# Performance work log

Measured on AMD Instinct MI355X. Metric: run time of the kernel, lower is better.

The kernel has to match this reference:

```python
import jax, jax.numpy as jnp
import numpy as np

D_MODEL = 1024
D_STATE = 16
D_CONV = 4
EXPAND = 2
D_INNER = EXPAND * D_MODEL  # 2048
DT_RANK = 64  # ceil(1024/16)
BATCH = 2
SEQ = 1024
EPS = 1e-5


def _causal_depthwise_conv(x, w, b):
    # x: (B, L, D); w: (D, K) depthwise kernel; b: (D,)
    K = w.shape[1]
    xp = jnp.pad(x, ((0, 0), (K - 1, 0), (0, 0)))            # left-pad for causality
    out = jax.lax.conv_general_dilated(
        xp.transpose(0, 2, 1),          # (B, D, L+K-1)
        w[:, None, :],                  # (D, 1, K)
        window_strides=(1,), padding='VALID',
        feature_group_count=w.shape[0])
    return out.transpose(0, 2, 1) + b   # (B, L, D)


def _ssm_dir(xs, conv_w, conv_b, xproj_w, dt_w, dt_b, A_log, D_skip):
    # xs: (B, L, D_INNER)
    Bsz = xs.shape[0]
    xc = jax.nn.silu(_causal_depthwise_conv(xs, conv_w, conv_b))
    x_dbl = xc @ xproj_w                                        # (B, L, dt_rank + 2N)
    dt, B_ssm, C_ssm = jnp.split(x_dbl, [DT_RANK, DT_RANK + D_STATE], axis=-1)
    dt = jax.nn.softplus(dt @ dt_w + dt_b)                      # (B, L, D_INNER)
    A = -jnp.exp(A_log)                                         # (D_INNER, N)
    dA = jnp.exp(dt[..., None] * A)                             # (B, L, D_INNER, N)
    dBu = dt[..., None] * B_ssm[:, :, None, :] * xc[..., None]  # (B, L, D_INNER, N)

    def step(h, inp):
        dAt, dBut, ct = inp          # (B,D,N), (B,D,N), (B,N)
        h = dAt * h + dBut
        y = jnp.einsum('bdn,bn->bd', h, ct)
        return h, y

    h0 = jnp.zeros((Bsz, D_INNER, D_STATE), dtype=xs.dtype)
    _, ys = jax.lax.scan(step, h0,
                         (jnp.moveaxis(dA, 1, 0), jnp.moveaxis(dBu, 1, 0), jnp.moveaxis(C_ssm, 1, 0)))
    y = jnp.moveaxis(ys, 0, 1)                                  # (B, L, D_INNER)
    return y + xc * D_skip


def _layernorm(x, gamma, beta):
    mu = jnp.mean(x, axis=-1, keepdims=True)
    var = jnp.mean(jnp.square(x - mu), axis=-1, keepdims=True)
    return (x - mu) * jax.lax.rsqrt(var + EPS) * gamma + beta


def setup_inputs() -> dict:
    key = jax.random.key(0)
    ks = jax.random.split(key, 24)
    s = 0.02
    A_init = jnp.log(jnp.tile(jnp.arange(1, D_STATE + 1, dtype=jnp.float32)[None, :], (D_INNER, 1)))
    # dt bias init (inverse-softplus of small dt), as in the torch module
    dt0 = jnp.exp(jax.random.uniform(ks[20], (D_INNER,)) * (np.log(0.1) - np.log(0.001)) + np.log(0.001))
    dt0 = jnp.clip(dt0, 1e-4)
    inv_dt = dt0 + jnp.log(-jnp.expm1(-dt0))
    return {
        'x': jax.random.normal(ks[0], (BATCH, SEQ, D_MODEL), jnp.float32),
        'gamma': jnp.ones((D_MODEL,), jnp.float32),
        'beta': jnp.zeros((D_MODEL,), jnp.float32),
        'in_w': jax.random.normal(ks[1], (D_MODEL, 2 * D_INNER), jnp.float32) * s,
        'conv_w': jax.random.normal(ks[2], (D_INNER, D_CONV), jnp.float32) * s,
        'conv_b': jnp.zeros((D_INNER,), jnp.float32),
        'xproj_w': jax.random.normal(ks[3], (D_INNER, DT_RANK + 2 * D_STATE), jnp.float32) * s,
        'dt_w': jax.random.normal(ks[4], (DT_RANK, D_INNER), jnp.float32) * s,
        'dt_b': inv_dt,
        'A_log': A_init,
        'D_skip': jnp.ones((D_INNER,), jnp.float32),
        'conv_w_b': jax.random.normal(ks[5], (D_INNER, D_CONV), jnp.float32) * s,
        'conv_b_b': jnp.zeros((D_INNER,), jnp.float32),
        'xproj_w_b': jax.random.normal(ks[6], (D_INNER, DT_RANK + 2 * D_STATE), jnp.float32) * s,
        'dt_w_b': jax.random.normal(ks[7], (DT_RANK, D_INNER), jnp.float32) * s,
        'dt_b_b': inv_dt,
        'A_log_b': A_init,
        'D_skip_b': jnp.ones((D_INNER,), jnp.float32),
        'merge_w': jax.random.normal(ks[8], (2 * D_INNER, D_INNER), jnp.float32) * s,
        'out_w': jax.random.normal(ks[9], (D_INNER, D_MODEL), jnp.float32) * s,
    }


def reference(x, gamma, beta, in_w, conv_w, conv_b, xproj_w, dt_w, dt_b, A_log, D_skip,
              conv_w_b, conv_b_b, xproj_w_b, dt_w_b, dt_b_b, A_log_b, D_skip_b,
              merge_w, out_w):
    residual = x
    h = _layernorm(x, gamma, beta)
    xz = h @ in_w                               # (B, L, 2*D_INNER)
    xs, z = jnp.split(xz, 2, axis=-1)
    y_fwd = _ssm_dir(xs, conv_w, conv_b, xproj_w, dt_w, dt_b, A_log, D_skip)
    y_back = _ssm_dir(xs[:, ::-1], conv_w_b, conv_b_b, xproj_w_b, dt_w_b, dt_b_b, A_log_b, D_skip_b)[:, ::-1]
    y = jnp.concatenate([y_fwd, y_back], axis=-1) @ merge_w
    y = y * jax.nn.silu(z)
    y = y @ out_w
    return residual + y
```

## Files before the change

### kernel.cpp

```cpp
#include <hip/hip_runtime.h>
#include <hip/hip_bf16.h>
#include <math.h>

typedef __hip_bfloat16 bf16;
typedef unsigned int u32;
typedef __attribute__((ext_vector_type(8))) short bf16x8;
typedef __attribute__((ext_vector_type(4))) float f32x4;

#define BATCH 2
#define SEQ 1024
#define DM 1024
#define DI 2048
#define NST 16
#define DTR 64
#define XDN 96
#define XDP_LD 128
#define T_TOK 2048
#define N2 4096
#define NCHUNK 32
#define CLEN 32

static __device__ __forceinline__ float b2f(bf16 v) { return __bfloat162float(v); }
static __device__ __forceinline__ float bits2f(unsigned short u) {
    return __uint_as_float(((unsigned)u) << 16);
}

static __device__ __forceinline__ float softplus_fast(float t) {
    return (t > 20.f) ? t : __logf(1.f + __expf(t));
}

static __device__ __forceinline__ void gload_lds16(const void* g, void* l) {
    __builtin_amdgcn_global_load_lds((__attribute__((address_space(1))) u32*)(size_t)g,
                                     (__attribute__((address_space(3))) u32*)l, 16, 0, 0);
}

#define SBAR() do { asm volatile("" ::: "memory"); __builtin_amdgcn_s_barrier(); asm volatile("" ::: "memory"); } while (0)

static __device__ void tileT(const float* __restrict__ in, bf16* __restrict__ out,
                             int K, int N, int t, float (*tb)[33]) {
    int nt = N >> 5;
    int bx = (t % nt) << 5, by = (t / nt) << 5;
    int tx = threadIdx.x & 31, r0 = threadIdx.x >> 5;
#pragma unroll
    for (int r = r0; r < 32; r += 8)
        tb[r][tx] = in[(size_t)(by + r) * N + bx + tx];
    __syncthreads();
#pragma unroll
    for (int r = r0; r < 32; r += 8)
        out[(size_t)(bx + r) * K + by + tx] = __float2bfloat16(tb[tx][r]);
}

#define LN_BLKS   T_TOK
#define INW_T     ((N2 / 32) * (DM / 32))
#define OUTW_T    ((DM / 32) * (DI / 32))
#define MRGW_T    ((DI / 32) * (N2 / 32))
#define SMALL_BLK ((2 * XDP_LD * DI + 2 * DI * DTR) / 256)

__global__ __launch_bounds__(256) void prep_mega(const float* __restrict__ x,
                                                 const float* __restrict__ gamma,
                                                 const float* __restrict__ beta,
                                                 bf16* __restrict__ H,
                                                 const float* __restrict__ in_w, bf16* __restrict__ in_wT,
                                                 const float* __restrict__ out_w, bf16* __restrict__ out_wT,
                                                 const float* __restrict__ merge_w, bf16* __restrict__ merge_wT,
                                                 const float* __restrict__ xpf, const float* __restrict__ xpb,
                                                 bf16* __restrict__ XPF, bf16* __restrict__ XPB,
                                                 const float* __restrict__ dtwf, const float* __restrict__ dtwb,
                                                 bf16* __restrict__ dtwT) {
    __shared__ float tbuf[32][33];
    __shared__ float red[8];
    int bid = blockIdx.x;
    int tid = threadIdx.x;

    if (bid < LN_BLKS) {
        int t = bid;
        float xv[4];
        float s = 0.f, s2 = 0.f;
#pragma unroll
        for (int k = 0; k < 4; ++k) {
            float v = x[(size_t)t * DM + k * 256 + tid];
            xv[k] = v; s += v; s2 += v * v;
        }
#pragma unroll
        for (int off = 32; off; off >>= 1) {
            s  += __shfl_down(s, off);
            s2 += __shfl_down(s2, off);
        }
        int wid = tid >> 6, lane = tid & 63;
        if (!lane) { red[wid] = s; red[4 + wid] = s2; }
        __syncthreads();
        if (tid == 0) {
            float S = red[0] + red[1] + red[2] + red[3];
            float S2 = red[4] + red[5] + red[6] + red[7];
            float mu = S * (1.f / DM);
            float var = S2 * (1.f / DM) - mu * mu;
            red[0] = mu;
            red[1] = rsqrtf(var + 1e-5f);
        }
        __syncthreads();
        float mu = red[0], rs = red[1];
#pragma unroll
        for (int k = 0; k < 4; ++k) {
            int i = k * 256 + tid;
            H[(size_t)t * DM + i] = __float2bfloat16((xv[k] - mu) * rs * gamma[i] + beta[i]);
        }
        return;
    }
    bid -= LN_BLKS;
    if (bid < INW_T)  { tileT(in_w, in_wT, DM, N2, bid, tbuf); return; }
    bid -= INW_T;
    if (bid < OUTW_T) { tileT(out_w, out_wT, DI, DM, bid, tbuf); return; }
    bid -= OUTW_T;
    if (bid < MRGW_T) { tileT(merge_w, merge_wT, N2, DI, bid, tbuf); return; }
    bid -= MRGW_T;
    int idx = bid * 256 + tid;
    if (idx < 2 * XDP_LD * DI) {
        int dir = idx >= XDP_LD * DI;
        int i = idx - dir * (XDP_LD * DI);
        int n = i >> 11;
        int k = i & (DI - 1);
        float v = (n < XDN) ? (dir ? xpb : xpf)[k * XDN + n] : 0.f;
        (dir ? XPB : XPF)[i] = __float2bfloat16(v);
    } else {
        int j = idx - 2 * XDP_LD * DI;
        int dir = j >= DI * DTR;
        int e = j - dir * (DI * DTR);
        int n = e >> 6;
        int k = e & 63;
        dtwT[(size_t)dir * DI * DTR + n * DTR + k] =
            __float2bfloat16((dir ? dtwb : dtwf)[(size_t)k * DI + n]);
    }
}

template <int EPI>
__global__ __launch_bounds__(256) void mfma_gemm(const bf16* __restrict__ A,
                                                 const bf16* __restrict__ BT,
                                                 const bf16* __restrict__ BT2, int bysplit,
                                                 bf16* __restrict__ Cb,
                                                 const float* __restrict__ resid,
                                                 float* __restrict__ outf,
                                                 bf16* __restrict__ Pb,
                                                 const float* __restrict__ bias1,
                                                 const float* __restrict__ bias2,
                                                 int M, int N, int K) {
    __shared__ bf16 As[8192];
    __shared__ bf16 Bs[8192];
    int tid = threadIdx.x;
    int wave = tid >> 6, lane = tid & 63;
    int q = lane >> 4, ln16 = lane & 15;
    int bm = blockIdx.y * 128, bn = blockIdx.x * 128;
    int wm = (wave >> 1) * 64, wn = (wave & 1) * 64;
    const bf16* Bt = ((int)blockIdx.y < bysplit) ? BT : BT2;

    int ks = K / gridDim.z;
    int kb = blockIdx.z * ks;

    f32x4 zf; zf[0] = zf[1] = zf[2] = zf[3] = 0.f;
    f32x4 acc[4][4];
#pragma unroll
    for (int i = 0; i < 4; ++i)
#pragma unroll
        for (int j = 0; j < 4; ++j) acc[i][j] = zf;

    for (int k0 = kb; k0 < kb + ks; k0 += 64) {
#pragma unroll
        for (int i = 0; i < 4; ++i) {
            int s = wave * 256 + i * 64 + lane;
            int kg = s >> 7, m = s & 127;
            gload_lds16(&A[(size_t)(bm + m) * K + k0 + kg * 8], &As[(wave * 256 + i * 64) * 8]);
            gload_lds16(&Bt[(size_t)(bn + m) * K + k0 + kg * 8], &Bs[(wave * 256 + i * 64) * 8]);
        }
        __syncthreads();
#pragma unroll
        for (int kk = 0; kk < 2; ++kk) {
            bf16x8 af[4], bfr[4];
#pragma unroll
            for (int i = 0; i < 4; ++i) {
                af[i]  = *(const bf16x8*)&As[(((kk * 4 + q) * 128) + (wm + i * 16 + ln16)) * 8];
                bfr[i] = *(const bf16x8*)&Bs[(((kk * 4 + q) * 128) + (wn + i * 16 + ln16)) * 8];
            }
#pragma unroll
            for (int i = 0; i < 4; ++i)
#pragma unroll
                for (int j = 0; j < 4; ++j)
                    acc[i][j] = __builtin_amdgcn_mfma_f32_16x16x32_bf16(af[i], bfr[j], acc[i][j], 0, 0, 0);
        }
        __syncthreads();
    }

    size_t pbase = (size_t)blockIdx.z * M * N;
#pragma unroll
    for (int i = 0; i < 4; ++i)
#pragma unroll
        for (int r = 0; r < 4; ++r) {
            int row = bm + wm + i * 16 + q * 4 + r;
            const float* bias = (EPI == 4) ? ((row < T_TOK) ? bias1 : bias2) : nullptr;
#pragma unroll
            for (int j = 0; j < 4; ++j) {
                int col = bn + wn + j * 16 + ln16;
                size_t idx = (size_t)row * N + col;
                float v = acc[i][j][r];
                if (EPI == 0)      Cb[idx] = __float2bfloat16(v);
                else if (EPI == 1) outf[idx] = resid[idx] + v;
                else if (EPI == 2) outf[idx] = v;
                else if (EPI == 3) Pb[pbase + idx] = __float2bfloat16(v);
                else {
                    Cb[idx] = __float2bfloat16(softplus_fast(v + bias[col]));
                }
            }
        }
}

template <int EPI>
__global__ __launch_bounds__(512, 2) void gemm256(const bf16* __restrict__ A,
                                                  const bf16* __restrict__ BT,
                                                  bf16* __restrict__ Cb,
                                                  bf16* __restrict__ Pb,
                                                  int M, int N, int K) {
    __shared__ bf16 LA[4][8192];
    __shared__ bf16 LB[4][8192];
    int tid = threadIdx.x;
    int wave = tid >> 6, lane = tid & 63;
    int q = lane >> 4, ln16 = lane & 15;

    int gx = gridDim.x, gy = gridDim.y, gz = gridDim.z;
    int L = blockIdx.x + gx * (blockIdx.y + gy * blockIdx.z);
    int nwg = gx * gy * gz;
    int qd = nwg >> 3, rd = nwg & 7;
    int xcd = L & 7, base = L >> 3;
    int wg = (xcd < rd ? xcd * (qd + 1) : rd * (qd + 1) + (xcd - rd) * qd) + base;
    int bxi = wg % gx, byi = (wg / gx) % gy, bzi = wg / (gx * gy);

    int bm = byi * 256, bn = bxi * 256;
    int wm = (wave >> 2) * 128, wn = (wave & 3) * 64;
    int ksz = K / gz;
    int kb = bzi * ksz;
    int NT = ksz >> 5;

    int o0 = tid * 16, o1 = 8192 + tid * 16;
    int r0 = o0 >> 6, r1 = o1 >> 6;
    int c0 = (o0 & 63) ^ (((r0 >> 1) & 3) << 4);
    int c1 = (o1 & 63) ^ (((r1 >> 1) & 3) << 4);
    const bf16* pa0 = &A[(size_t)(bm + r0) * K + kb + (c0 >> 1)];
    const bf16* pa1 = &A[(size_t)(bm + r1) * K + kb + (c1 >> 1)];
    const bf16* pb0 = &BT[(size_t)(bn + r0) * K + kb + (c0 >> 1)];
    const bf16* pb1 = &BT[(size_t)(bn + r1) * K + kb + (c1 >> 1)];
    int d0 = wave * 512;
    int d1 = 4096 + wave * 512;

    int aoff[8], boff[4];
#pragma unroll
    for (int i = 0; i < 8; ++i) {
        int r = wm + i * 16 + ln16;
        aoff[i] = (r * 64 + q * 16) ^ (((r >> 1) & 3) << 4);
    }
#pragma unroll
    for (int j = 0; j < 4; ++j) {
        int r = wn + j * 16 + ln16;
        boff[j] = (r * 64 + q * 16) ^ (((r >> 1) & 3) << 4);
    }

    f32x4 zf; zf[0] = zf[1] = zf[2] = zf[3] = 0.f;
    f32x4 acc[8][4];
#pragma unroll
    for (int i = 0; i < 8; ++i)
#pragma unroll
        for (int j = 0; j < 4; ++j) acc[i][j] = zf;

    auto STAGE = [&](int b, int koff) {
        gload_lds16(pa0 + koff, &LA[b][d0]);
        gload_lds16(pa1 + koff, &LA[b][d1]);
        gload_lds16(pb0 + koff, &LB[b][d0]);
        gload_lds16(pb1 + koff, &LB[b][d1]);
    };

#define RD_FRAGS(AV, BV, TT) do {                                             \
        const bf16* LAb_ = LA[(TT) & 3];                                      \
        const bf16* LBb_ = LB[(TT) & 3];                                      \
        _Pragma("unroll")                                                     \
        for (int j_ = 0; j_ < 4; ++j_) BV[j_] = *(const bf16x8*)&LBb_[boff[j_] >> 1]; \
        _Pragma("unroll")                                                     \
        for (int i_ = 0; i_ < 8; ++i_) AV[i_] = *(const bf16x8*)&LAb_[aoff[i_] >> 1]; \
    } while (0)

#define MFMA_ALL(AV, BV) do {                                                 \
        __builtin_amdgcn_s_setprio(1);                                        \
        _Pragma("unroll")                                                     \
        for (int i_ = 0; i_ < 8; ++i_)                                        \
            _Pragma("unroll")                                                 \
            for (int j_ = 0; j_ < 4; ++j_)                                    \
                acc[i_][j_] = __builtin_amdgcn_mfma_f32_16x16x32_bf16(AV[i_], BV[j_], acc[i_][j_], 0, 0, 0); \
        __builtin_amdgcn_s_setprio(0);                                        \
    } while (0)

    bf16x8 avX[8], bvX[4], avY[8], bvY[4];

    STAGE(0, 0); STAGE(1, 32); STAGE(2, 64);
    asm volatile("s_waitcnt vmcnt(4)" ::: "memory");
    SBAR();
    RD_FRAGS(avX, bvX, 0);

    for (int t = 0; t < NT; t += 2) {
        if (t + 1 < NT) RD_FRAGS(avY, bvY, t + 1);
        if (t + 3 < NT) STAGE((t + 3) & 3, (t + 3) * 32);
        MFMA_ALL(avX, bvX);
        if (t + 3 < NT)      asm volatile("s_waitcnt vmcnt(4)" ::: "memory");
        else if (t + 2 < NT) asm volatile("s_waitcnt vmcnt(0)" ::: "memory");
        SBAR();
        if (t + 2 < NT) RD_FRAGS(avX, bvX, t + 2);
        if (t + 4 < NT) STAGE((t + 4) & 3, (t + 4) * 32);
        MFMA_ALL(avY, bvY);
        if (t + 4 < NT)      asm volatile("s_waitcnt vmcnt(4)" ::: "memory");
        else if (t + 3 < NT) asm volatile("s_waitcnt vmcnt(0)" ::: "memory");
        SBAR();
    }
#undef RD_FRAGS
#undef MFMA_ALL

    size_t pbase = (size_t)bzi * ((size_t)M * N);
#pragma unroll
    for (int i = 0; i < 8; ++i)
#pragma unroll
        for (int r = 0; r < 4; ++r) {
            int row = bm + wm + i * 16 + q * 4 + r;
#pragma unroll
            for (int j = 0; j < 4; ++j) {
                int col = bn + wn + j * 16 + ln16;
                size_t idx = (size_t)row * N + col;
                float v = acc[i][j][r];
                if (EPI == 0) Cb[idx] = __float2bfloat16(v);
                else          Pb[pbase + idx] = __float2bfloat16(v);
            }
        }
}

__global__ __launch_bounds__(256) void reduce_plain(const bf16* __restrict__ P, int ns, size_t MN,
                                                    bf16* __restrict__ O) {
    size_t i = ((size_t)blockIdx.x * 256 + threadIdx.x) * 4;
    float s[4] = {0.f, 0.f, 0.f, 0.f};
    for (int k = 0; k < ns; ++k) {
        ushort4 p = *reinterpret_cast<const ushort4*>(&P[(size_t)k * MN + i]);
        s[0] += bits2f(p.x); s[1] += bits2f(p.y); s[2] += bits2f(p.z); s[3] += bits2f(p.w);
    }
    bf16 r[4];
#pragma unroll
    for (int j = 0; j < 4; ++j) r[j] = __float2bfloat16(s[j]);
    *reinterpret_cast<ushort4*>(&O[i]) = *reinterpret_cast<ushort4*>(r);
}

__global__ __launch_bounds__(256) void reduce_gate(const bf16* __restrict__ P, int ns, size_t MN,
                                                   const bf16* __restrict__ XZ, bf16* __restrict__ YM) {
    size_t i = ((size_t)blockIdx.x * 256 + threadIdx.x) * 4;
    float s[4] = {0.f, 0.f, 0.f, 0.f};
    for (int k = 0; k < ns; ++k) {
        ushort4 p = *reinterpret_cast<const ushort4*>(&P[(size_t)k * MN + i]);
        s[0] += bits2f(p.x); s[1] += bits2f(p.y); s[2] += bits2f(p.z); s[3] += bits2f(p.w);
    }
    int t = (int)(i >> 11), c = (int)(i & (DI - 1));
    const bf16* zp = &XZ[(size_t)t * N2 + DI + c];
    bf16 r[4];
#pragma unroll
    for (int j = 0; j < 4; ++j) {
        float z = b2f(zp[j]);
        r[j] = __float2bfloat16(s[j] * (z / (1.f + __expf(-z))));
    }
    *reinterpret_cast<ushort4*>(&YM[i]) = *reinterpret_cast<ushort4*>(r);
}

__global__ __launch_bounds__(256) void reduce_out(const bf16* __restrict__ P, int ns, size_t MN,
                                                  const float* __restrict__ x, float* __restrict__ out) {
    size_t i = ((size_t)blockIdx.x * 256 + threadIdx.x) * 4;
    float s[4] = {0.f, 0.f, 0.f, 0.f};
    for (int k = 0; k < ns; ++k) {
        ushort4 p = *reinterpret_cast<const ushort4*>(&P[(size_t)k * MN + i]);
        s[0] += bits2f(p.x); s[1] += bits2f(p.y); s[2] += bits2f(p.z); s[3] += bits2f(p.w);
    }
    float4 xv = *reinterpret_cast<const float4*>(&x[i]);
    float4 o = {s[0] + xv.x, s[1] + xv.y, s[2] + xv.z, s[3] + xv.w};
    *reinterpret_cast<float4*>(&out[i]) = o;
}

__global__ __launch_bounds__(256) void reduce_xdbl(const bf16* __restrict__ P, int ns, size_t MN,
                                                   float* __restrict__ XDP, bf16* __restrict__ XDdt) {
    size_t i = ((size_t)blockIdx.x * 256 + threadIdx.x) * 4;
    float s[4] = {0.f, 0.f, 0.f, 0.f};
    for (int k = 0; k < ns; ++k) {
        ushort4 p = *reinterpret_cast<const ushort4*>(&P[(size_t)k * MN + i]);
        s[0] += bits2f(p.x); s[1] += bits2f(p.y); s[2] += bits2f(p.z); s[3] += bits2f(p.w);
    }
    float4 o = {s[0], s[1], s[2], s[3]};
    *reinterpret_cast<float4*>(&XDP[i]) = o;
    int col = (int)(i & (XDP_LD - 1));
    if (col < DTR) {
        size_t row = i >> 7;
        bf16 r[4];
#pragma unroll
        for (int j = 0; j < 4; ++j) r[j] = __float2bfloat16(s[j]);
        *reinterpret_cast<ushort4*>(&XDdt[row * DTR + col]) = *reinterpret_cast<ushort4*>(r);
    }
}

__global__ __launch_bounds__(256) void gemm_dt(const float* __restrict__ A,
                                               const float* __restrict__ Bw,
                                               const float* __restrict__ bias,
                                               bf16* __restrict__ Cb, int M, int N) {
    __shared__ float As[16][68];
    __shared__ float Bs[16][68];
    int tid = threadIdx.x;
    int bm = blockIdx.y * 64, bn = blockIdx.x * 64;
    int tx = tid & 15, ty = tid >> 4;
    float acc[4][4];
#pragma unroll
    for (int i = 0; i < 4; ++i)
#pragma unroll
        for (int j = 0; j < 4; ++j) acc[i][j] = 0.f;
    int arow = tid >> 2, acg = (tid & 3) * 4;
    int brow = tid >> 4, bcol = (tid & 15) * 4;
    for (int k0 = 0; k0 < DTR; k0 += 16) {
        float4 av = *reinterpret_cast<const float4*>(&A[(size_t)(bm + arow) * XDP_LD + k0 + acg]);
        As[acg + 0][arow] = av.x; As[acg + 1][arow] = av.y;
        As[acg + 2][arow] = av.z; As[acg + 3][arow] = av.w;
        float4 bv = *reinterpret_cast<const float4*>(&Bw[(size_t)(k0 + brow) * N + bn + bcol]);
        Bs[brow][bcol + 0] = bv.x; Bs[brow][bcol + 1] = bv.y;
        Bs[brow][bcol + 2] = bv.z; Bs[brow][bcol + 3] = bv.w;
        __syncthreads();
#pragma unroll
        for (int kk = 0; kk < 16; ++kk) {
            float4 a = *reinterpret_cast<const float4*>(&As[kk][ty * 4]);
            float4 b = *reinterpret_cast<const float4*>(&Bs[kk][tx * 4]);
            acc[0][0] += a.x * b.x; acc[0][1] += a.x * b.y; acc[0][2] += a.x * b.z; acc[0][3] += a.x * b.w;
            acc[1][0] += a.y * b.x; acc[1][1] += a.y * b.y; acc[1][2] += a.y * b.z; acc[1][3] += a.y * b.w;
            acc[2][0] += a.z * b.x; acc[2][1] += a.z * b.y; acc[2][2] += a.z * b.z; acc[2][3] += a.z * b.w;
            acc[3][0] += a.w * b.x; acc[3][1] += a.w * b.y; acc[3][2] += a.w * b.z; acc[3][3] += a.w * b.w;
        }
        __syncthreads();
    }
    int row0 = bm + ty * 4, col0 = bn + tx * 4;
#pragma unroll
    for (int i = 0; i < 4; ++i)
#pragma unroll
        for (int j = 0; j < 4; ++j) {
            float v = acc[i][j] + bias[col0 + j];
            Cb[(size_t)(row0 + i) * N + col0 + j] = __float2bfloat16(softplus_fast(v));
        }
}

__global__ __launch_bounds__(256) void conv_kernel(const bf16* __restrict__ XZ,
                                                   const float* __restrict__ wf, const float* __restrict__ bf_,
                                                   const float* __restrict__ wb, const float* __restrict__ bb_,
                                                   bf16* __restrict__ XCF, bf16* __restrict__ XCB) {
    int idx = blockIdx.x * 256 + threadIdx.x;
    int c = idx & (DI - 1);
    int g = idx >> 11;
    int l = g & (SEQ - 1);
    int b = g >> 10;
    float sf = bf_[c];
    float sb = bb_[c];
#pragma unroll
    for (int j = 0; j < 4; ++j) {
        int lf = l - 3 + j;
        if (lf >= 0) sf += wf[c * 4 + j] * b2f(XZ[((size_t)(b * SEQ + lf)) * N2 + c]);
        int lb = l + 3 - j;
        if (lb < SEQ) sb += wb[c * 4 + j] * b2f(XZ[((size_t)(b * SEQ + lb)) * N2 + c]);
    }
    XCF[idx] = __float2bfloat16(sf / (1.f + __expf(-sf)));
    XCB[idx] = __float2bfloat16(sb / (1.f + __expf(-sb)));
}

template <bool FINAL>
__global__ __launch_bounds__(256) void scan_chunk(const bf16* __restrict__ DTF_, const bf16* __restrict__ DTB_,
                                                  const bf16* __restrict__ XCF_, const bf16* __restrict__ XCB_,
                                                  const float* __restrict__ XDP,
                                                  const float* __restrict__ Af, const float* __restrict__ Ab,
                                                  const float* __restrict__ Df, const float* __restrict__ Db,
                                                  float* __restrict__ HLOC, float* __restrict__ SUMDT,
                                                  bf16* __restrict__ YCAT) {
    __shared__ float bsl[CLEN][32];
    int tid = threadIdx.x;
    int sg = tid & 1;
    int c = blockIdx.x * 128 + (tid >> 1);
    int b = blockIdx.y;
    int dir = blockIdx.z >> 5, chunk = blockIdx.z & 31;
    {
        int it = tid >> 3, j4 = (tid & 7) * 4;
        int sit = chunk * CLEN + it;
        int l = dir ? (SEQ - 1 - sit) : sit;
        size_t row = (size_t)dir * T_TOK + (size_t)b * SEQ + l;
        *(float4*)&bsl[it][j4] = *(const float4*)&XDP[row * XDP_LD + DTR + j4];
    }
    const bf16* DT = dir ? DTB_ : DTF_;
    const bf16* XC = dir ? XCB_ : XCF_;
    const float* Al = dir ? Ab : Af;
    float A[8];
#pragma unroll
    for (int n = 0; n < 8; ++n) A[n] = -__expf(Al[c * NST + sg * 8 + n]);
    size_t base = ((((size_t)dir * BATCH + b) * NCHUNK + chunk) * DI + c);
    float h[8];
    float Dv = 0.f;
    if (FINAL) {
#pragma unroll
        for (int n = 0; n < 8; ++n) h[n] = HLOC[base * NST + sg * 8 + n];
        Dv = (dir ? Db : Df)[c];
    } else {
#pragma unroll
        for (int n = 0; n < 8; ++n) h[n] = 0.f;
    }
    __syncthreads();
    float sumdt = 0.f;
    for (int it = 0; it < CLEN; ++it) {
        int sit = chunk * CLEN + it;
        int l = dir ? (SEQ - 1 - sit) : sit;
        size_t g = (size_t)b * SEQ + l;
        float dt = b2f(DT[g * DI + c]);
        float xc = b2f(XC[g * DI + c]);
        float dtxc = dt * xc;
        const float* bs = &bsl[it][sg * 8];
        if (FINAL) {
            float y = 0.f;
#pragma unroll
            for (int n = 0; n < 8; ++n) {
                h[n] = __expf(dt * A[n]) * h[n] + dtxc * bs[n];
                y += h[n] * bs[NST + n];
            }
            y += __shfl_xor(y, 1);
            if (!sg) YCAT[g * N2 + dir * DI + c] = __float2bfloat16(y + xc * Dv);
        } else {
            sumdt += dt;
#pragma unroll
            for (int n = 0; n < 8; ++n)
                h[n] = __expf(dt * A[n]) * h[n] + dtxc * bs[n];
        }
    }
    if (!FINAL) {
#pragma unroll
        for (int n = 0; n < 8; ++n) HLOC[base * NST + sg * 8 + n] = h[n];
        if (!sg) SUMDT[base] = sumdt;
    }
}

__global__ __launch_bounds__(256) void scan_combine(float* __restrict__ HLOC,
                                                    const float* __restrict__ SUMDT,
                                                    const float* __restrict__ Af,
                                                    const float* __restrict__ Ab) {
    int idx = blockIdx.x * 256 + threadIdx.x;
    int n = idx & 15;
    int c = (idx >> 4) & (DI - 1);
    int b = (idx >> 15) & 1;
    int dir = idx >> 16;
    float A = -__expf((dir ? Ab : Af)[c * NST + n]);
    float h = 0.f;
    for (int k = 0; k < NCHUNK; ++k) {
        size_t base = ((((size_t)dir * BATCH + b) * NCHUNK + k) * DI + c);
        float P = __expf(A * SUMDT[base]);
        float hl = HLOC[base * NST + n];
        HLOC[base * NST + n] = h;
        h = P * h + hl;
    }
}

__global__ __launch_bounds__(256) void gate_kernel(bf16* __restrict__ YM, const bf16* __restrict__ XZ) {
    int idx = blockIdx.x * 256 + threadIdx.x;
    int t = idx >> 11;
    int c = idx & (DI - 1);
    float z = b2f(XZ[(size_t)t * N2 + DI + c]);
    float y = b2f(YM[idx]);
    YM[idx] = __float2bfloat16(y * (z / (1.f + __expf(-z))));
}

extern "C" void kernel_launch(void* const* d_in, const int* in_sizes, int n_in,
                              void* d_out, int out_size, void* d_ws, size_t ws_size,
                              hipStream_t stream) {
    const float* x       = (const float*)d_in[0];
    const float* gamma   = (const float*)d_in[1];
    const float* beta    = (const float*)d_in[2];
    const float* in_w    = (const float*)d_in[3];
    const float* conv_w  = (const float*)d_in[4];
    const float* conv_b  = (const float*)d_in[5];
    const float* xproj_w = (const float*)d_in[6];
    const float* dt_w    = (const float*)d_in[7];
    const float* dt_b    = (const float*)d_in[8];
    const float* A_log   = (const float*)d_in[9];
    const float* D_skip  = (const float*)d_in[10];
    const float* conv_w_b  = (const float*)d_in[11];
    const float* conv_b_b  = (const float*)d_in[12];
    const float* xproj_w_b = (const float*)d_in[13];
    const float* dt_w_b    = (const float*)d_in[14];
    const float* dt_b_b    = (const float*)d_in[15];
    const float* A_log_b   = (const float*)d_in[16];
    const float* D_skip_b  = (const float*)d_in[17];
    const float* merge_w   = (const float*)d_in[18];
    const float* out_w     = (const float*)d_in[19];
    float* out = (float*)d_out;

    char* w = (char*)d_ws;
    size_t off = 0;
    bf16* H       = (bf16*)(w + off); off += (size_t)T_TOK * DM * 2;
    bf16* XZ      = (bf16*)(w + off); off += (size_t)T_TOK * N2 * 2;
    bf16* XCF     = (bf16*)(w + off); off += (size_t)T_TOK * DI * 2;
    bf16* XCB     = (bf16*)(w + off); off += (size_t)T_TOK * DI * 2;
    bf16* XPF     = (bf16*)(w + off); off += (size_t)XDP_LD * DI * 2;
    bf16* XPB     = (bf16*)(w + off); off += (size_t)XDP_LD * DI * 2;
    float* XDP    = (float*)(w + off); off += (size_t)2 * T_TOK * XDP_LD * 4;
    bf16* DTF     = (bf16*)(w + off); off += (size_t)T_TOK * DI * 2;
    bf16* DTB     = (bf16*)(w + off); off += (size_t)T_TOK * DI * 2;
    bf16* YCAT    = (bf16*)(w + off); off += (size_t)T_TOK * N2 * 2;
    bf16* in_wT   = (bf16*)(w + off); off += (size_t)N2 * DM * 2;
    bf16* out_wT  = (bf16*)(w + off); off += (size_t)DM * DI * 2;
    bf16* merge_wT= (bf16*)(w + off); off += (size_t)DI * N2 * 2;
    bf16* dtwT    = (bf16*)(w + off); off += (size_t)2 * DI * DTR * 2;
    bf16* XDdt    = (bf16*)(w + off); off += (size_t)2 * T_TOK * DTR * 2;
    char* PART = w + off;
    size_t avail = (ws_size > off) ? ws_size - off : 0;

    float* HLOC  = (float*)PART;
    float* SUMDT = (float*)(PART + (size_t)2 * BATCH * NCHUNK * DI * NST * 4);
    bf16* Pb     = (bf16*)PART;
    bf16* YM     = DTF;

    size_t MNm = (size_t)T_TOK * DI;
    size_t MNo = (size_t)T_TOK * DM;
    size_t MNx = (size_t)2 * T_TOK * XDP_LD;
    size_t MNz = (size_t)T_TOK * N2;
    int s_merge = (avail >= 4 * MNm * 2) ? 4 : (avail >= 2 * MNm * 2) ? 2 : 0;
    int s_out   = (avail >= 4 * MNo * 2) ? 4 : (avail >= 2 * MNo * 2) ? 2 : 0;
    int s_xdbl  = (avail >= 16 * MNx * 2) ? 16 : (avail >= 8 * MNx * 2) ? 8 : (avail >= 4 * MNx * 2) ? 4 : 0;
    int s_xz    = (avail >= 2 * MNz * 2) ? 2 : 0;

    prep_mega<<<LN_BLKS + INW_T + OUTW_T + MRGW_T + SMALL_BLK, 256, 0, stream>>>(
        x, gamma, beta, H, in_w, in_wT, out_w, out_wT, merge_w, merge_wT,
        xproj_w, xproj_w_b, XPF, XPB, dt_w, dt_w_b, dtwT);
    if (s_xz) {
        gemm256<3><<<dim3(N2 / 256, T_TOK / 256, s_xz), 512, 0, stream>>>(
            H, in_wT, nullptr, Pb, T_TOK, N2, DM);
        reduce_plain<<<(int)(MNz / 4 / 256), 256, 0, stream>>>(Pb, s_xz, MNz, XZ);
    } else {
        mfma_gemm<0><<<dim3(N2 / 128, T_TOK / 128), 256, 0, stream>>>(
            H, in_wT, in_wT, 1 << 30, XZ, nullptr, nullptr, nullptr, nullptr, nullptr, T_TOK, N2, DM);
    }
    conv_kernel<<<(T_TOK * DI) / 256, 256, 0, stream>>>(XZ, conv_w, conv_b, conv_w_b, conv_b_b, XCF, XCB);
    if (s_xdbl) {
        mfma_gemm<3><<<dim3(1, (2 * T_TOK) / 128, s_xdbl), 256, 0, stream>>>(
            XCF, XPF, XPB, (T_TOK / 128), nullptr, nullptr, nullptr, Pb, nullptr, nullptr,
            2 * T_TOK, XDP_LD, DI);
        reduce_xdbl<<<(int)(MNx / 4 / 256), 256, 0, stream>>>(Pb, s_xdbl, MNx, XDP, XDdt);
        mfma_gemm<4><<<dim3(DI / 128, (2 * T_TOK) / 128), 256, 0, stream>>>(
            XDdt, dtwT, dtwT + (size_t)DI * DTR, (T_TOK / 128), DTF, nullptr, nullptr, nullptr,
            dt_b, dt_b_b, 2 * T_TOK, DI, DTR);
    } else {
        mfma_gemm<2><<<dim3(1, (2 * T_TOK) / 128), 256, 0, stream>>>(
            XCF, XPF, XPB, (T_TOK / 128), nullptr, nullptr, XDP, nullptr, nullptr, nullptr,
            2 * T_TOK, XDP_LD, DI);
        gemm_dt<<<dim3(DI / 64, T_TOK / 64), 256, 0, stream>>>(XDP, dt_w, dt_b, DTF, T_TOK, DI);
        gemm_dt<<<dim3(DI / 64, T_TOK / 64), 256, 0, stream>>>(XDP + (size_t)T_TOK * XDP_LD, dt_w_b, dt_b_b, DTB, T_TOK, DI);
    }
    scan_chunk<false><<<dim3(DI / 128, BATCH, 2 * NCHUNK), 256, 0, stream>>>(
        DTF, DTB, XCF, XCB, XDP, A_log, A_log_b, D_skip, D_skip_b, HLOC, SUMDT, YCAT);
    scan_combine<<<(2 * BATCH * DI * NST) / 256, 256, 0, stream>>>(HLOC, SUMDT, A_log, A_log_b);
    scan_chunk<true><<<dim3(DI / 128, BATCH, 2 * NCHUNK), 256, 0, stream>>>(
        DTF, DTB, XCF, XCB, XDP, A_log, A_log_b, D_skip, D_skip_b, HLOC, SUMDT, YCAT);
    if (s_merge) {
        gemm256<3><<<dim3(DI / 256, T_TOK / 256, s_merge), 512, 0, stream>>>(
            YCAT, merge_wT, nullptr, Pb, T_TOK, DI, N2);
        reduce_gate<<<(int)(MNm / 4 / 256), 256, 0, stream>>>(Pb, s_merge, MNm, XZ, YM);
    } else {
        mfma_gemm<0><<<dim3(DI / 128, T_TOK / 128), 256, 0, stream>>>(
            YCAT, merge_wT, merge_wT, 1 << 30, YM, nullptr, nullptr, nullptr, nullptr, nullptr,
            T_TOK, DI, N2);
        gate_kernel<<<(T_TOK * DI) / 256, 256, 0, stream>>>(YM, XZ);
    }
    if (s_out) {
        mfma_gemm<3><<<dim3(DM / 128, T_TOK / 128, s_out), 256, 0, stream>>>(
            YM, out_wT, out_wT, 1 << 30, nullptr, nullptr, nullptr, Pb, nullptr, nullptr,
            T_TOK, DM, DI);
        reduce_out<<<(int)(MNo / 4 / 256), 256, 0, stream>>>(Pb, s_out, MNo, x, out);
    } else {
        mfma_gemm<1><<<dim3(DM / 128, T_TOK / 128), 256, 0, stream>>>(
            YM, out_wT, out_wT, 1 << 30, nullptr, x, out, nullptr, nullptr, nullptr,
            T_TOK, DM, DI);
    }
}
```

Baseline: 400.0 us.

## Restructure gemm256 to 64-wide K double-buffer with interleaved staging; stage scan inputs in LDS

```diff
diff --git a/kernel.cpp b/kernel.cpp
--- a/kernel.cpp
+++ b/kernel.cpp
@@ -217,8 +217,8 @@
                                                   bf16* __restrict__ Cb,
                                                   bf16* __restrict__ Pb,
                                                   int M, int N, int K) {
-    __shared__ bf16 LA[4][8192];
-    __shared__ bf16 LB[4][8192];
+    __shared__ bf16 LA[2][16384];
+    __shared__ bf16 LB[2][16384];
     int tid = threadIdx.x;
     int wave = tid >> 6, lane = tid & 63;
     int q = lane >> 4, ln16 = lane & 15;
@@ -235,30 +235,21 @@
     int wm = (wave >> 2) * 128, wn = (wave & 3) * 64;
     int ksz = K / gz;
     int kb = bzi * ksz;
-    int NT = ksz >> 5;
-
-    int o0 = tid * 16, o1 = 8192 + tid * 16;
-    int r0 = o0 >> 6, r1 = o1 >> 6;
-    int c0 = (o0 & 63) ^ (((r0 >> 1) & 3) << 4);
-    int c1 = (o1 & 63) ^ (((r1 >> 1) & 3) << 4);
-    const bf16* pa0 = &A[(size_t)(bm + r0) * K + kb + (c0 >> 1)];
-    const bf16* pa1 = &A[(size_t)(bm + r1) * K + kb + (c1 >> 1)];
-    const bf16* pb0 = &BT[(size_t)(bn + r0) * K + kb + (c0 >> 1)];
-    const bf16* pb1 = &BT[(size_t)(bn + r1) * K + kb + (c1 >> 1)];
-    int d0 = wave * 512;
-    int d1 = 4096 + wave * 512;
-
-    int aoff[8], boff[4];
-#pragma unroll
-    for (int i = 0; i < 8; ++i) {
-        int r = wm + i * 16 + ln16;
-        aoff[i] = (r * 64 + q * 16) ^ (((r >> 1) & 3) << 4);
-    }
-#pragma unroll
-    for (int j = 0; j < 4; ++j) {
-        int r = wn + j * 16 + ln16;
-        boff[j] = (r * 64 + q * 16) ^ (((r >> 1) & 3) << 4);
-    }
+    int NT64 = ksz >> 6;
+    int NIT = NT64 >> 1;
+
+    int row_off = tid >> 3;
+    int csrc = (tid & 7) ^ (row_off & 7);
+    const bf16* pa = &A[(size_t)(bm + row_off) * K + kb + csrc * 8];
+    const bf16* pb = &BT[(size_t)(bn + row_off) * K + kb + csrc * 8];
+    size_t s64K = (size_t)64 * K;
+    int dls = wave * 512;
+
+    int m3 = ln16 & 7;
+    int c0 = (q ^ m3) * 8;
+    int c1 = ((4 + q) ^ m3) * 8;
+    int abase = (wm + ln16) * 64;
+    int bbase = (wn + ln16) * 64;
 
     f32x4 zf; zf[0] = zf[1] = zf[2] = zf[3] = 0.f;
     f32x4 acc[8][4];
@@ -267,55 +258,79 @@
 #pragma unroll
         for (int j = 0; j < 4; ++j) acc[i][j] = zf;
 
-    auto STAGE = [&](int b, int koff) {
-        gload_lds16(pa0 + koff, &LA[b][d0]);
-        gload_lds16(pa1 + koff, &LA[b][d1]);
-        gload_lds16(pb0 + koff, &LB[b][d0]);
-        gload_lds16(pb1 + koff, &LB[b][d1]);
-    };
-
-#define RD_FRAGS(AV, BV, TT) do {                                             \
-        const bf16* LAb_ = LA[(TT) & 3];                                      \
-        const bf16* LBb_ = LB[(TT) & 3];                                      \
+#define STG_A(buf, t, half) do {                                              \
+        const bf16* s_ = pa + (size_t)(t) * 64 + (size_t)((half) * 2) * s64K; \
+        gload_lds16(s_,        &LA[buf][(half) * 8192 + dls]);                \
+        gload_lds16(s_ + s64K, &LA[buf][(half) * 8192 + 4096 + dls]);         \
+    } while (0)
+#define STG_B(buf, t, half) do {                                              \
+        const bf16* s_ = pb + (size_t)(t) * 64 + (size_t)((half) * 2) * s64K; \
+        gload_lds16(s_,        &LB[buf][(half) * 8192 + dls]);                \
+        gload_lds16(s_ + s64K, &LB[buf][(half) * 8192 + 4096 + dls]);         \
+    } while (0)
+#define RD_A(LAP, I0, CC)                                                     \
         _Pragma("unroll")                                                     \
-        for (int j_ = 0; j_ < 4; ++j_) BV[j_] = *(const bf16x8*)&LBb_[boff[j_] >> 1]; \
+        for (int u_ = 0; u_ < 4; ++u_)                                        \
+            a0[u_] = *(const bf16x8*)&LAP[abase + ((I0) + u_) * 1024 + (CC)];
+#define RD_B(DST, LBP, CC)                                                    \
         _Pragma("unroll")                                                     \
-        for (int i_ = 0; i_ < 8; ++i_) AV[i_] = *(const bf16x8*)&LAb_[aoff[i_] >> 1]; \
-    } while (0)
-
-#define MFMA_ALL(AV, BV) do {                                                 \
+        for (int u_ = 0; u_ < 4; ++u_)                                        \
+            DST[u_] = *(const bf16x8*)&LBP[bbase + u_ * 1024 + (CC)];
+#define MQ(I0, BV) do {                                                       \
         __builtin_amdgcn_s_setprio(1);                                        \
         _Pragma("unroll")                                                     \
-        for (int i_ = 0; i_ < 8; ++i_)                                        \
+        for (int i_ = 0; i_ < 4; ++i_)                                        \
             _Pragma("unroll")                                                 \
             for (int j_ = 0; j_ < 4; ++j_)                                    \
-                acc[i_][j_] = __builtin_amdgcn_mfma_f32_16x16x32_bf16(AV[i_], BV[j_], acc[i_][j_], 0, 0, 0); \
+                acc[(I0) + i_][j_] = __builtin_amdgcn_mfma_f32_16x16x32_bf16( \
+                    a0[i_], BV[j_], acc[(I0) + i_][j_], 0, 0, 0);             \
         __builtin_amdgcn_s_setprio(0);                                        \
     } while (0)
 
-    bf16x8 avX[8], bvX[4], avY[8], bvY[4];
-
-    STAGE(0, 0); STAGE(1, 32); STAGE(2, 64);
+    bf16x8 a0[4], b0[4], b1[4];
+
+    STG_A(0, 0, 0); STG_A(0, 0, 1);
+    STG_B(0, 0, 0); STG_B(0, 0, 1);
+    STG_B(1, 1, 0); STG_B(1, 1, 1);
     asm volatile("s_waitcnt vmcnt(4)" ::: "memory");
     SBAR();
-    RD_FRAGS(avX, bvX, 0);
-
-    for (int t = 0; t < NT; t += 2) {
-        if (t + 1 < NT) RD_FRAGS(avY, bvY, t + 1);
-        if (t + 3 < NT) STAGE((t + 3) & 3, (t + 3) * 32);
-        MFMA_ALL(avX, bvX);
-        if (t + 3 < NT)      asm volatile("s_waitcnt vmcnt(4)" ::: "memory");
-        else if (t + 2 < NT) asm volatile("s_waitcnt vmcnt(0)" ::: "memory");
-        SBAR();
-        if (t + 2 < NT) RD_FRAGS(avX, bvX, t + 2);
-        if (t + 4 < NT) STAGE((t + 4) & 3, (t + 4) * 32);
-        MFMA_ALL(avY, bvY);
-        if (t + 4 < NT)      asm volatile("s_waitcnt vmcnt(4)" ::: "memory");
-        else if (t + 3 < NT) asm volatile("s_waitcnt vmcnt(0)" ::: "memory");
-        SBAR();
-    }
-#undef RD_FRAGS
-#undef MFMA_ALL
+
+    for (int j = 0; j < NIT; ++j) {
+        int ta = 2 * j, tb = ta + 1;
+        bool st = (j + 1 < NIT);
+        const bf16* A0 = LA[0]; const bf16* B0 = LB[0];
+        const bf16* A1 = LA[1]; const bf16* B1 = LB[1];
+        RD_B(b0, B0, c0); RD_B(b1, B0, c1); RD_A(A0, 0, c0);
+        STG_A(1, tb, 0);
+        SBAR(); MQ(0, b0); SBAR();
+        RD_A(A0, 0, c1);
+        STG_A(1, tb, 1);
+        SBAR(); MQ(0, b1); SBAR();
+        RD_A(A0, 4, c0);
+        if (st) STG_B(0, ta + 2, 0);
+        SBAR(); MQ(4, b0); SBAR();
+        RD_A(A0, 4, c1);
+        if (st) { STG_B(0, ta + 2, 1); asm volatile("s_waitcnt vmcnt(4)" ::: "memory"); }
+        else    { asm volatile("s_waitcnt vmcnt(0)" ::: "memory"); }
+        SBAR(); MQ(4, b1); SBAR();
+        RD_B(b0, B1, c0); RD_B(b1, B1, c1); RD_A(A1, 0, c0);
+        if (st) STG_A(0, ta + 2, 0);
+        SBAR(); MQ(0, b0); SBAR();
+        RD_A(A1, 0, c1);
+        if (st) STG_A(0, ta + 2, 1);
+        SBAR(); MQ(0, b1); SBAR();
+        RD_A(A1, 4, c0);
+        if (st) STG_B(1, tb + 2, 0);
+        SBAR(); MQ(4, b0); SBAR();
+        RD_A(A1, 4, c1);
+        if (st) { STG_B(1, tb + 2, 1); asm volatile("s_waitcnt vmcnt(4)" ::: "memory"); }
+        SBAR(); MQ(4, b1); SBAR();
+    }
+#undef STG_A
+#undef STG_B
+#undef RD_A
+#undef RD_B
+#undef MQ
 
     size_t pbase = (size_t)bzi * ((size_t)M * N);
 #pragma unroll
@@ -476,11 +491,17 @@
                                                   float* __restrict__ HLOC, float* __restrict__ SUMDT,
                                                   bf16* __restrict__ YCAT) {
     __shared__ float bsl[CLEN][32];
+    __shared__ bf16 dtl[CLEN][128];
+    __shared__ bf16 xcl[CLEN][128];
     int tid = threadIdx.x;
     int sg = tid & 1;
-    int c = blockIdx.x * 128 + (tid >> 1);
+    int cl = tid >> 1;
+    int cbase = blockIdx.x * 128;
+    int c = cbase + cl;
     int b = blockIdx.y;
     int dir = blockIdx.z >> 5, chunk = blockIdx.z & 31;
+    const bf16* DT = dir ? DTB_ : DTF_;
+    const bf16* XC = dir ? XCB_ : XCF_;
     {
         int it = tid >> 3, j4 = (tid & 7) * 4;
         int sit = chunk * CLEN + it;
@@ -488,8 +509,14 @@
         size_t row = (size_t)dir * T_TOK + (size_t)b * SEQ + l;
         *(float4*)&bsl[it][j4] = *(const float4*)&XDP[row * XDP_LD + DTR + j4];
     }
-    const bf16* DT = dir ? DTB_ : DTF_;
-    const bf16* XC = dir ? XCB_ : XCF_;
+    for (int ch = tid; ch < 512; ch += 256) {
+        int it = ch >> 4, of = (ch & 15) * 8;
+        int sit = chunk * CLEN + it;
+        int l = dir ? (SEQ - 1 - sit) : sit;
+        size_t g = (size_t)b * SEQ + l;
+        *(bf16x8*)&dtl[it][of] = *(const bf16x8*)&DT[g * DI + cbase + of];
+        *(bf16x8*)&xcl[it][of] = *(const bf16x8*)&XC[g * DI + cbase + of];
+    }
     const float* Al = dir ? Ab : Af;
     float A[8];
 #pragma unroll
@@ -511,8 +538,8 @@
         int sit = chunk * CLEN + it;
         int l = dir ? (SEQ - 1 - sit) : sit;
         size_t g = (size_t)b * SEQ + l;
-        float dt = b2f(DT[g * DI + c]);
-        float xc = b2f(XC[g * DI + c]);
+        float dt = b2f(dtl[it][cl]);
+        float xc = b2f(xcl[it][cl]);
         float dtxc = dt * xc;
         const float* bs = &bsl[it][sg * 8];
         if (FINAL) {
```

Result: no change. 399.4 us (-0.2%).

## Stage dt/xc tiles in LDS and double scan chunk count

Applied to the files above, without the earlier changes.

```diff
diff --git a/kernel.cpp b/kernel.cpp
--- a/kernel.cpp
+++ b/kernel.cpp
@@ -17,8 +17,6 @@
 #define XDP_LD 128
 #define T_TOK 2048
 #define N2 4096
-#define NCHUNK 32
-#define CLEN 32
 
 static __device__ __forceinline__ float b2f(bf16 v) { return __bfloat162float(v); }
 static __device__ __forceinline__ float bits2f(unsigned short u) {
@@ -467,7 +465,7 @@
     XCB[idx] = __float2bfloat16(sb / (1.f + __expf(-sb)));
 }
 
-template <bool FINAL>
+template <int NC, bool FINAL>
 __global__ __launch_bounds__(256) void scan_chunk(const bf16* __restrict__ DTF_, const bf16* __restrict__ DTB_,
                                                   const bf16* __restrict__ XCF_, const bf16* __restrict__ XCB_,
                                                   const float* __restrict__ XDP,
@@ -475,26 +473,40 @@
                                                   const float* __restrict__ Df, const float* __restrict__ Db,
                                                   float* __restrict__ HLOC, float* __restrict__ SUMDT,
                                                   bf16* __restrict__ YCAT) {
-    __shared__ float bsl[CLEN][32];
+    constexpr int CL = SEQ / NC;
+    __shared__ float bsl[CL][32];
+    __shared__ bf16 dtl[CL][128];
+    __shared__ bf16 xcl[CL][128];
     int tid = threadIdx.x;
     int sg = tid & 1;
-    int c = blockIdx.x * 128 + (tid >> 1);
+    int cl = tid >> 1;
+    int cbase = blockIdx.x * 128;
+    int c = cbase + cl;
     int b = blockIdx.y;
-    int dir = blockIdx.z >> 5, chunk = blockIdx.z & 31;
-    {
-        int it = tid >> 3, j4 = (tid & 7) * 4;
-        int sit = chunk * CLEN + it;
+    int dir = (int)blockIdx.z >= NC;
+    int chunk = blockIdx.z - dir * NC;
+    const bf16* DT = dir ? DTB_ : DTF_;
+    const bf16* XC = dir ? XCB_ : XCF_;
+    for (int i = tid; i < CL * 8; i += 256) {
+        int it = i >> 3, j4 = (i & 7) * 4;
+        int sit = chunk * CL + it;
         int l = dir ? (SEQ - 1 - sit) : sit;
         size_t row = (size_t)dir * T_TOK + (size_t)b * SEQ + l;
         *(float4*)&bsl[it][j4] = *(const float4*)&XDP[row * XDP_LD + DTR + j4];
     }
-    const bf16* DT = dir ? DTB_ : DTF_;
-    const bf16* XC = dir ? XCB_ : XCF_;
+    for (int ch = tid; ch < CL * 16; ch += 256) {
+        int it = ch >> 4, of = (ch & 15) * 8;
+        int sit = chunk * CL + it;
+        int l = dir ? (SEQ - 1 - sit) : sit;
+        size_t g = (size_t)b * SEQ + l;
+        *(bf16x8*)&dtl[it][of] = *(const bf16x8*)&DT[g * DI + cbase + of];
+        *(bf16x8*)&xcl[it][of] = *(const bf16x8*)&XC[g * DI + cbase + of];
+    }
     const float* Al = dir ? Ab : Af;
     float A[8];
 #pragma unroll
     for (int n = 0; n < 8; ++n) A[n] = -__expf(Al[c * NST + sg * 8 + n]);
-    size_t base = ((((size_t)dir * BATCH + b) * NCHUNK + chunk) * DI + c);
+    size_t base = ((((size_t)dir * BATCH + b) * NC + chunk) * DI + c);
     float h[8];
     float Dv = 0.f;
     if (FINAL) {
@@ -507,12 +519,12 @@
     }
     __syncthreads();
     float sumdt = 0.f;
-    for (int it = 0; it < CLEN; ++it) {
-        int sit = chunk * CLEN + it;
+    for (int it = 0; it < CL; ++it) {
+        int sit = chunk * CL + it;
         int l = dir ? (SEQ - 1 - sit) : sit;
         size_t g = (size_t)b * SEQ + l;
-        float dt = b2f(DT[g * DI + c]);
-        float xc = b2f(XC[g * DI + c]);
+        float dt = b2f(dtl[it][cl]);
+        float xc = b2f(xcl[it][cl]);
         float dtxc = dt * xc;
         const float* bs = &bsl[it][sg * 8];
         if (FINAL) {
@@ -541,7 +553,7 @@
 __global__ __launch_bounds__(256) void scan_combine(float* __restrict__ HLOC,
                                                     const float* __restrict__ SUMDT,
                                                     const float* __restrict__ Af,
-                                                    const float* __restrict__ Ab) {
+                                                    const float* __restrict__ Ab, int nchunk) {
     int idx = blockIdx.x * 256 + threadIdx.x;
     int n = idx & 15;
     int c = (idx >> 4) & (DI - 1);
@@ -549,8 +561,8 @@
     int dir = idx >> 16;
     float A = -__expf((dir ? Ab : Af)[c * NST + n]);
     float h = 0.f;
-    for (int k = 0; k < NCHUNK; ++k) {
-        size_t base = ((((size_t)dir * BATCH + b) * NCHUNK + k) * DI + c);
+    for (int k = 0; k < nchunk; ++k) {
+        size_t base = ((((size_t)dir * BATCH + b) * nchunk + k) * DI + c);
         float P = __expf(A * SUMDT[base]);
         float hl = HLOC[base * NST + n];
         HLOC[base * NST + n] = h;
@@ -612,8 +624,10 @@
     char* PART = w + off;
     size_t avail = (ws_size > off) ? ws_size - off : 0;
 
+    size_t need64 = (size_t)2 * BATCH * 64 * DI * NST * 4 + (size_t)2 * BATCH * 64 * DI * 4;
+    int nchunk = (avail >= need64) ? 64 : 32;
     float* HLOC  = (float*)PART;
-    float* SUMDT = (float*)(PART + (size_t)2 * BATCH * NCHUNK * DI * NST * 4);
+    float* SUMDT = (float*)(PART + (size_t)2 * BATCH * nchunk * DI * NST * 4);
     bf16* Pb     = (bf16*)PART;
     bf16* YM     = DTF;
 
@@ -653,11 +667,19 @@
         gemm_dt<<<dim3(DI / 64, T_TOK / 64), 256, 0, stream>>>(XDP, dt_w, dt_b, DTF, T_TOK, DI);
         gemm_dt<<<dim3(DI / 64, T_TOK / 64), 256, 0, stream>>>(XDP + (size_t)T_TOK * XDP_LD, dt_w_b, dt_b_b, DTB, T_TOK, DI);
     }
-    scan_chunk<false><<<dim3(DI / 128, BATCH, 2 * NCHUNK), 256, 0, stream>>>(
-        DTF, DTB, XCF, XCB, XDP, A_log, A_log_b, D_skip, D_skip_b, HLOC, SUMDT, YCAT);
-    scan_combine<<<(2 * BATCH * DI * NST) / 256, 256, 0, stream>>>(HLOC, SUMDT, A_log, A_log_b);
-    scan_chunk<true><<<dim3(DI / 128, BATCH, 2 * NCHUNK), 256, 0, stream>>>(
-        DTF, DTB, XCF, XCB, XDP, A_log, A_log_b, D_skip, D_skip_b, HLOC, SUMDT, YCAT);
+    if (nchunk == 64) {
+        scan_chunk<64, false><<<dim3(DI / 128, BATCH, 128), 256, 0, stream>>>(
+            DTF, DTB, XCF, XCB, XDP, A_log, A_log_b, D_skip, D_skip_b, HLOC, SUMDT, YCAT);
+        scan_combine<<<(2 * BATCH * DI * NST) / 256, 256, 0, stream>>>(HLOC, SUMDT, A_log, A_log_b, 64);
+        scan_chunk<64, true><<<dim3(DI / 128, BATCH, 128), 256, 0, stream>>>(
+            DTF, DTB, XCF, XCB, XDP, A_log, A_log_b, D_skip, D_skip_b, HLOC, SUMDT, YCAT);
+    } else {
+        scan_chunk<32, false><<<dim3(DI / 128, BATCH, 64), 256, 0, stream>>>(
+            DTF, DTB, XCF, XCB, XDP, A_log, A_log_b, D_skip, D_skip_b, HLOC, SUMDT, YCAT);
+        scan_combine<<<(2 * BATCH * DI * NST) / 256, 256, 0, stream>>>(HLOC, SUMDT, A_log, A_log_b, 32);
+        scan_chunk<32, true><<<dim3(DI / 128, BATCH, 64), 256, 0, stream>>>(
+            DTF, DTB, XCF, XCB, XDP, A_log, A_log_b, D_skip, D_skip_b, HLOC, SUMDT, YCAT);
+    }
     if (s_merge) {
         gemm256<3><<<dim3(DI / 256, T_TOK / 256, s_merge), 512, 0, stream>>>(
             YCAT, merge_wT, nullptr, Pb, T_TOK, DI, N2);
```

Result: slower. 408.5 us (+2.1%).
